# Optimization experiments

Measured on AMD Instinct MI355X. Metric: run time of the kernel, lower is better.

## Reference

```python
import jax, jax.numpy as jnp
import numpy as np

N = 50000   # nodes
E = 400000  # edges
R = 35      # num_relations
B = 12      # num_bases
C = 128     # hidden_conv_dim (heads=1)
T = 4       # node types: load, gen, load_gen, ext
HL = 38     # hidden_lin_dim
OUT = 2


def setup_inputs() -> dict:
    key = jax.random.key(0)
    ks = jax.random.split(key, 24)
    s = 0.1  # param scale
    inp = {
        'x': jax.random.normal(ks[0], (N, 2), jnp.float32),
        'edge_index': jax.random.randint(ks[1], (2, E), 0, N, jnp.int32),
        'edge_type': jax.random.randint(ks[2], (E,), 0, R, jnp.int32),
        'edge_attr': jax.random.normal(ks[3], (E, 2), jnp.float32),
        'node_type': jax.random.randint(ks[4], (N,), 0, T, jnp.int32),
        'basis': jax.random.normal(ks[5], (B, 2, C), jnp.float32) * s,
        'att_rel': jax.random.normal(ks[6], (R, B), jnp.float32) * s,
        'q_att': jax.random.normal(ks[7], (C, 1), jnp.float32) * s,
        'k_att': jax.random.normal(ks[8], (C, 1), jnp.float32) * s,
        'e_att': jax.random.normal(ks[9], (C, 1), jnp.float32) * s,
        'lin_edge_W': jax.random.normal(ks[10], (2, C), jnp.float32) * s,
        'conv_bias': jax.random.normal(ks[11], (C,), jnp.float32) * s,
        'lin0_W': jax.random.normal(ks[12], (T, C, HL), jnp.float32) * s,
        'lin0_b': jax.random.normal(ks[13], (T, HL), jnp.float32) * s,
        'lin1_W': jax.random.normal(ks[14], (T, HL, HL), jnp.float32) * s,
        'lin1_b': jax.random.normal(ks[15], (T, HL), jnp.float32) * s,
        'lin2_W': jax.random.normal(ks[16], (T, HL, HL), jnp.float32) * s,
        'lin2_b': jax.random.normal(ks[17], (T, HL), jnp.float32) * s,
        'fin_W': jax.random.normal(ks[18], (T, HL, OUT), jnp.float32) * s,
        'fin_b': jax.random.normal(ks[19], (T, OUT), jnp.float32) * s,
    }
    return inp


def _segment_softmax(alpha, dst, n):
    # PyG softmax: max is detached, eps=1e-16 on the denominator
    amax = jax.lax.stop_gradient(jax.ops.segment_max(alpha, dst, num_segments=n))
    ex = jnp.exp(alpha - amax[dst])
    den = jax.ops.segment_sum(ex, dst, num_segments=n) + 1e-16
    return ex / den[dst]


def _per_type_linear(xv, W, b, t):
    # apply node-type-specific Linear: [N,d] x [T,d,h] -> pick row type
    y = jnp.einsum('nd,tdh->nth', xv, W)              # [N,T,h]
    y = jnp.take_along_axis(y, t[:, None, None], axis=1)[:, 0]
    return y + b[t]


def reference(x, edge_index, edge_type, edge_attr, node_type,
              basis, att_rel, q_att, k_att, e_att, lin_edge_W, conv_bias,
              lin0_W, lin0_b, lin1_W, lin1_b, lin2_W, lin2_b, fin_W, fin_b):
    n = x.shape[0]
    src, dst = edge_index[0], edge_index[1]
    # RGATConv with basis decomposition: per-relation weight [R, in=2, C]
    w = jnp.einsum('rb,bio->rio', att_rel, basis)
    w_e = w[edge_type]                                 # [E,2,C] edge gather
    out_i = jnp.einsum('ei,eic->ec', x[dst], w_e)      # [E,C]
    out_j = jnp.einsum('ei,eic->ec', x[src], w_e)      # [E,C]
    ke = (edge_attr @ lin_edge_W) @ e_att              # [E,1]
    alpha = out_i @ q_att + out_j @ k_att + ke         # additive self-attention
    alpha = jax.nn.leaky_relu(alpha, 0.2)
    alpha = _segment_softmax(alpha, dst, n)            # across-relation segment softmax
    msg = alpha * out_j                                # heads=1 -> [E,C]
    agg = jax.ops.segment_sum(msg, dst, num_segments=n) + conv_bias
    h = jax.nn.leaky_relu(agg, 0.2)                    # forward activation (dropout: eval)
    t = node_type
    h = _per_type_linear(jax.nn.relu(h), lin0_W, lin0_b, t)
    h = _per_type_linear(jax.nn.relu(h), lin1_W, lin1_b, t)
    h = _per_type_linear(jax.nn.relu(h), lin2_W, lin2_b, t)
    out = _per_type_linear(h, fin_W, fin_b, t)         # [N,2]
    # load nodes (type 0): second output passes through abs
    load_out = jnp.concatenate([out[:, :1], jnp.abs(out[:, 1:2])], axis=1)
    return jnp.where((t == 0)[:, None], load_out, out)
```

## Files before the change

### kernel.cpp

```cpp
#include <hip/hip_runtime.h>
#include <math.h>

#define N_NODES 50000
#define N_EDGES 400000
#define R_REL   35
#define B_BASES 12
#define C_DIM   128
#define HL_DIM  38
#define RI2     70
#define NP      50304
#define NB_HIST 196
#define NBUCK   786
#define EPB     2048
#define CAP     704

#define OFF_WT     0
#define OFF_WQ     8960
#define OFF_WK     9030
#define OFF_LE     9100
#define OFF_META   9104
#define OFF_HBLK   9120
#define OFF_PERM   10688
#define OFF_INV    60688
#define OFF_ECUR   110992
#define OFF_EREC   111780

#define ST    0
#define WT    4760
#define HH    0
#define Y0T   0
#define Y1T   3264
#define Y2T   0
#define W1S   8192
#define W2S   9720
#define W0F   13720
#define SM_DINV 18888
#define SM_FW   18952
#define SM_FB   19028
#define LDS_FLOATS 19030

__global__ __launch_bounds__(256) void k_init(const int* __restrict__ node_type,
                                              const float* __restrict__ basis,
                                              const float* __restrict__ att_rel,
                                              const float* __restrict__ q_att,
                                              const float* __restrict__ k_att,
                                              const float* __restrict__ e_att,
                                              const float* __restrict__ lin_edge_W,
                                              float* __restrict__ ws) {
    int b = blockIdx.x, tid = threadIdx.x;
    if (b < NB_HIST) {
        __shared__ int lh[4];
        if (tid < 4) lh[tid] = 0;
        __syncthreads();
        int i = b * 256 + tid;
        if (i < N_NODES) atomicAdd(&lh[node_type[i]], 1);
        __syncthreads();
        if (tid < 4) ((int*)(ws + OFF_HBLK))[b * 4 + tid] = lh[tid];
    } else if (b < NB_HIST + 35) {
        int idx = (b - NB_HIST) * 256 + tid;
        if (idx < RI2 * C_DIM) {
            int c  = idx & (C_DIM - 1);
            int ri = idx >> 7;
            int r = ri >> 1, ii = ri & 1;
            float acc = 0.f;
            #pragma unroll
            for (int bb = 0; bb < B_BASES; ++bb)
                acc += att_rel[r * B_BASES + bb] * basis[(bb * 2 + ii) * C_DIM + c];
            ws[OFF_WT + idx] = acc;
        }
    } else if (b == NB_HIST + 35) {
        for (int i = tid; i < NBUCK; i += 256) ((int*)(ws + OFF_ECUR))[i] = 0;
    } else {
        int lane = tid & 63, wv = tid >> 6;
        int u = (b - (NB_HIST + 36)) * 4 + wv;
        if (u < 2 * RI2) {
            int ri = (u < RI2) ? u : (u - RI2);
            int r = ri >> 1, ii = ri & 1;
            const float* av = att_rel + r * B_BASES;
            const float* bs = basis + ii * C_DIM;
            float w1 = 0.f, w2 = 0.f;
            #pragma unroll
            for (int bb = 0; bb < B_BASES; ++bb) {
                float a = av[bb];
                w1 += a * bs[bb * 2 * C_DIM + lane];
                w2 += a * bs[bb * 2 * C_DIM + 64 + lane];
            }
            const float* qk = (u < RI2) ? q_att : k_att;
            float s = w1 * qk[lane] + w2 * qk[64 + lane];
            #pragma unroll
            for (int off = 32; off; off >>= 1) s += __shfl_xor(s, off, 64);
            if (lane == 0) ws[((u < RI2) ? OFF_WQ : OFF_WK) + ri] = s;
        } else if (u < 2 * RI2 + 2) {
            int j = u - 2 * RI2;
            const float* er = lin_edge_W + j * C_DIM;
            float s = er[lane] * e_att[lane] + er[64 + lane] * e_att[64 + lane];
            #pragma unroll
            for (int off = 32; off; off >>= 1) s += __shfl_xor(s, off, 64);
            if (lane == 0) ws[OFF_LE + j] = s;
        }
    }
}

__global__ __launch_bounds__(256) void k_perm(const int* __restrict__ node_type,
                                              float* __restrict__ ws) {
    __shared__ int lh[NB_HIST * 4];
    __shared__ int pre[4], tot[4], basel[4];
    __shared__ int wcnt[4][4];
    int tid = threadIdx.x;
    int lane = tid & 63, wv = tid >> 6;
    const int* hblk = (const int*)(ws + OFF_HBLK);
    for (int i = tid; i < NB_HIST * 4; i += 256) lh[i] = hblk[i];
    __syncthreads();
    if (tid < 4) {
        int run = 0, mypre = 0;
        for (int bb = 0; bb < NB_HIST; ++bb) {
            if (bb == (int)blockIdx.x) mypre = run;
            run += lh[bb * 4 + tid];
        }
        pre[tid] = mypre;
        tot[tid] = run;
    }
    __syncthreads();
    if (tid == 0) {
        int t0 = tot[0], t1 = tot[1], t2 = tot[2];
        int b1 = ((t0 + 63) >> 6) << 6;
        int b2 = b1 + (((t1 + 63) >> 6) << 6);
        int b3 = b2 + (((t2 + 63) >> 6) << 6);
        basel[0] = 0; basel[1] = b1; basel[2] = b2; basel[3] = b3;
        if (blockIdx.x == 0) {
            int* meta = (int*)(ws + OFF_META);
            meta[0] = t0; meta[1] = t1; meta[2] = t2; meta[3] = tot[3];
            meta[4] = 0;  meta[5] = b1; meta[6] = b2; meta[7] = b3;
        }
    }
    __syncthreads();
    int n = blockIdx.x * 256 + tid;
    bool active = n < N_NODES;
    int ty = active ? node_type[n] : -1;
    int myrank = 0;
    #pragma unroll
    for (int t = 0; t < 4; ++t) {
        unsigned long long m = __ballot(ty == t);
        if (lane == 0) wcnt[wv][t] = __popcll(m);
        if (ty == t) myrank = __popcll(m & ((1ULL << lane) - 1ULL));
    }
    __syncthreads();
    if (active) {
        int prew = 0;
        for (int w2 = 0; w2 < wv; ++w2) prew += wcnt[w2][ty];
        int p = basel[ty] + pre[ty] + prew + myrank;
        ((int*)(ws + OFF_PERM))[n] = p;
        ((int*)(ws + OFF_INV))[p] = n;
    }
}

__global__ __launch_bounds__(256) void k_escatter(const float* __restrict__ x,
                                                  const int* __restrict__ edge_index,
                                                  const int* __restrict__ edge_type,
                                                  const float* __restrict__ edge_attr,
                                                  float* __restrict__ ws) {
    __shared__ int hist[NBUCK];
    __shared__ int sbase[NBUCK];
    __shared__ float swq[RI2], swk[RI2], sle[2];
    int tid = threadIdx.x;
    for (int i = tid; i < NBUCK; i += 256) hist[i] = 0;
    if (tid < RI2) { swq[tid] = ws[OFF_WQ + tid]; swk[tid] = ws[OFF_WK + tid]; }
    if (tid < 2) sle[tid] = ws[OFF_LE + tid];
    __syncthreads();

    const int* perm = (const int*)(ws + OFF_PERM);
    int base = blockIdx.x * EPB;
    int   rb[8], rm[8];
    float rex[8], rsx[8], rsy[8];
    #pragma unroll
    for (int k = 0; k < 8; ++k) {
        int e = base + k * 256 + tid;
        rb[k] = -1;
        if (e < N_EDGES) {
            int src = edge_index[e];
            int dst = edge_index[N_EDGES + e];
            int r   = edge_type[e];
            int p   = perm[dst];
            float2 ea = *(const float2*)(edge_attr + 2 * e);
            float2 xs = *(const float2*)(x + 2 * src);
            float2 xd = *(const float2*)(x + 2 * dst);
            float alpha = xd.x * swq[2 * r] + xd.y * swq[2 * r + 1]
                        + xs.x * swk[2 * r] + xs.y * swk[2 * r + 1]
                        + ea.x * sle[0]     + ea.y * sle[1];
            alpha = alpha > 0.f ? alpha : 0.2f * alpha;
            float ex = __expf(alpha);
            rb[k]  = p >> 6;
            rm[k]  = (r << 6) | (p & 63);
            rex[k] = ex;
            rsx[k] = ex * xs.x;
            rsy[k] = ex * xs.y;
            atomicAdd(&hist[rb[k]], 1);
        }
    }
    __syncthreads();
    int* gcur = (int*)(ws + OFF_ECUR);
    for (int i = tid; i < NBUCK; i += 256) {
        int c = hist[i];
        sbase[i] = (c > 0) ? atomicAdd(&gcur[i], c) : 0;
    }
    __syncthreads();
    float4* rec = (float4*)(ws + OFF_EREC);
    #pragma unroll
    for (int k = 0; k < 8; ++k) {
        if (rb[k] >= 0) {
            int slot = atomicAdd(&sbase[rb[k]], 1);
            rec[(size_t)rb[k] * CAP + slot] =
                make_float4(__int_as_float(rm[k]), rex[k], rsx[k], rsy[k]);
        }
    }
}

__global__ __launch_bounds__(256) void k_node(
        const float* __restrict__ ws, const float* __restrict__ conv_bias,
        const float* __restrict__ lin0_W, const float* __restrict__ lin0_b,
        const float* __restrict__ lin1_W, const float* __restrict__ lin1_b,
        const float* __restrict__ lin2_W, const float* __restrict__ lin2_b,
        const float* __restrict__ fin_W,  const float* __restrict__ fin_b,
        float* __restrict__ out) {
    __shared__ float L[LDS_FLOATS];
    int tid  = threadIdx.x;
    int lane = tid & 63;
    int wv   = tid >> 6;
    int p0   = blockIdx.x * 64;

    const int* meta = (const int*)(ws + OFF_META);
    int b1 = meta[5], b2 = meta[6], b3 = meta[7];
    int t  = (p0 >= b1) + (p0 >= b2) + (p0 >= b3);
    int bp = meta[4 + t];
    int cnt = meta[t];

    for (int i = tid; i < RI2 * 68; i += 256) L[ST + i] = 0.f;
    if (tid < 64) L[SM_DINV + tid] = 0.f;
    if (tid >= 64 && tid < 142) {
        int i = tid - 64;
        if (i < 76) L[SM_FW + i] = fin_W[t * 76 + i];
        else        L[SM_FB + i - 76] = fin_b[t * 2 + i - 76];
    }
    const float* wT_g = ws + OFF_WT;
    for (int i4 = tid; i4 < 2240; i4 += 256) {
        float4 v = ((const float4*)wT_g)[i4];
        *(float4*)&L[WT + i4 * 4] = v;
    }
    const float* W0g = lin0_W + t * C_DIM * HL_DIM;
    for (int i = tid; i < C_DIM * HL_DIM; i += 256) {
        int cc = i / 38, j = i - cc * 38;
        L[W0F + cc * 40 + j] = W0g[i];
    }
    __syncthreads();

    {
        int ecnt = ((const int*)(ws + OFF_ECUR))[blockIdx.x];
        const float4* rec = (const float4*)(ws + OFF_EREC) + (size_t)blockIdx.x * CAP;
        for (int i = tid; i < ecnt; i += 256) {
            float4 v = rec[i];
            int m = __float_as_int(v.x);
            int n = m & 63, r = m >> 6;
            atomicAdd(&L[ST + (2 * r) * 68 + n],     v.z);
            atomicAdd(&L[ST + (2 * r + 1) * 68 + n], v.w);
            atomicAdd(&L[SM_DINV + n],               v.y);
        }
    }
    __syncthreads();
    if (tid < 64) L[SM_DINV + tid] = 1.0f / (L[SM_DINV + tid] + 1e-16f);

    int ng = lane & 15, cg_ = lane >> 4;
    int c0 = wv * 32 + cg_ * 8;
    float acc[32];
    #pragma unroll
    for (int i = 0; i < 32; ++i) acc[i] = 0.f;
    #pragma unroll 5
    for (int kk = 0; kk < RI2; ++kk) {
        float4 a4 = *(const float4*)&L[ST + kk * 68 + ng * 4];
        float4 wa = *(const float4*)&L[WT + kk * 128 + c0];
        float4 wc = *(const float4*)&L[WT + kk * 128 + c0 + 4];
        float a_[4] = {a4.x, a4.y, a4.z, a4.w};
        float w_[8] = {wa.x, wa.y, wa.z, wa.w, wc.x, wc.y, wc.z, wc.w};
        #pragma unroll
        for (int ni = 0; ni < 4; ++ni)
            #pragma unroll
            for (int ci = 0; ci < 8; ++ci)
                acc[ni * 8 + ci] += a_[ni] * w_[ci];
    }
    __syncthreads();

    {
        float4 dv = *(const float4*)&L[SM_DINV + ng * 4];
        float d_[4] = {dv.x, dv.y, dv.z, dv.w};
        #pragma unroll
        for (int ci = 0; ci < 8; ++ci) {
            float cb = conv_bias[c0 + ci];
            float4 hv;
            float h0 = acc[0 * 8 + ci] * d_[0] + cb;
            float h1 = acc[1 * 8 + ci] * d_[1] + cb;
            float h2 = acc[2 * 8 + ci] * d_[2] + cb;
            float h3 = acc[3 * 8 + ci] * d_[3] + cb;
            hv.x = h0 > 0.f ? h0 : 0.f;
            hv.y = h1 > 0.f ? h1 : 0.f;
            hv.z = h2 > 0.f ? h2 : 0.f;
            hv.w = h3 > 0.f ? h3 : 0.f;
            *(float4*)&L[HH + (c0 + ci) * 64 + ng * 4] = hv;
        }
    }
    {
        const float* W1g = lin1_W + t * HL_DIM * HL_DIM;
        const float* W2g = lin2_W + t * HL_DIM * HL_DIM;
        for (int i = tid; i < HL_DIM * HL_DIM; i += 256) {
            int cc = i / 38, j = i - cc * 38;
            L[W1S + cc * 40 + j] = W1g[i];
            L[W2S + cc * 40 + j] = W2g[i];
        }
    }
    __syncthreads();

    int jg = lane >> 4;
    int j0 = wv * 16 + jg * 4;
    float acc2[16];
    #pragma unroll
    for (int i = 0; i < 16; ++i) acc2[i] = 0.f;
    if (wv < 3) {
        #pragma unroll 4
        for (int kk = 0; kk < C_DIM; ++kk) {
            float4 a4 = *(const float4*)&L[HH + kk * 64 + ng * 4];
            float4 w4 = *(const float4*)&L[W0F + kk * 40 + j0];
            float a_[4] = {a4.x, a4.y, a4.z, a4.w};
            float w_[4] = {w4.x, w4.y, w4.z, w4.w};
            #pragma unroll
            for (int ni = 0; ni < 4; ++ni)
                #pragma unroll
                for (int ji = 0; ji < 4; ++ji)
                    acc2[ni * 4 + ji] += a_[ni] * w_[ji];
        }
    }
    __syncthreads();

    if (wv < 3) {
        #pragma unroll
        for (int ji = 0; ji < 4; ++ji) {
            int j = j0 + ji;
            float b = (j < HL_DIM) ? lin0_b[t * HL_DIM + j] : 0.f;
            float4 yv;
            float y0 = acc2[0 * 4 + ji] + b;
            float y1 = acc2[1 * 4 + ji] + b;
            float y2 = acc2[2 * 4 + ji] + b;
            float y3 = acc2[3 * 4 + ji] + b;
            yv.x = y0 > 0.f ? y0 : 0.f;
            yv.y = y1 > 0.f ? y1 : 0.f;
            yv.z = y2 > 0.f ? y2 : 0.f;
            yv.w = y3 > 0.f ? y3 : 0.f;
            *(float4*)&L[Y0T + j * 68 + ng * 4] = yv;
        }
    }
    __syncthreads();

    if (wv < 3) {
        float acc3[16];
        #pragma unroll
        for (int i = 0; i < 16; ++i) acc3[i] = 0.f;
        #pragma unroll 2
        for (int kk = 0; kk < HL_DIM; ++kk) {
            float4 a4 = *(const float4*)&L[Y0T + kk * 68 + ng * 4];
            float4 w4 = *(const float4*)&L[W1S + kk * 40 + j0];
            float a_[4] = {a4.x, a4.y, a4.z, a4.w};
            float w_[4] = {w4.x, w4.y, w4.z, w4.w};
            #pragma unroll
            for (int ni = 0; ni < 4; ++ni)
                #pragma unroll
                for (int ji = 0; ji < 4; ++ji)
                    acc3[ni * 4 + ji] += a_[ni] * w_[ji];
        }
        #pragma unroll
        for (int ji = 0; ji < 4; ++ji) {
            int j = j0 + ji;
            float b = (j < HL_DIM) ? lin1_b[t * HL_DIM + j] : 0.f;
            float4 yv;
            float y0 = acc3[0 * 4 + ji] + b;
            float y1 = acc3[1 * 4 + ji] + b;
            float y2 = acc3[2 * 4 + ji] + b;
            float y3 = acc3[3 * 4 + ji] + b;
            yv.x = y0 > 0.f ? y0 : 0.f;
            yv.y = y1 > 0.f ? y1 : 0.f;
            yv.z = y2 > 0.f ? y2 : 0.f;
            yv.w = y3 > 0.f ? y3 : 0.f;
            *(float4*)&L[Y1T + j * 68 + ng * 4] = yv;
        }
    }
    __syncthreads();

    if (wv < 3) {
        float acc4[16];
        #pragma unroll
        for (int i = 0; i < 16; ++i) acc4[i] = 0.f;
        #pragma unroll 2
        for (int kk = 0; kk < HL_DIM; ++kk) {
            float4 a4 = *(const float4*)&L[Y1T + kk * 68 + ng * 4];
            float4 w4 = *(const float4*)&L[W2S + kk * 40 + j0];
            float a_[4] = {a4.x, a4.y, a4.z, a4.w};
            float w_[4] = {w4.x, w4.y, w4.z, w4.w};
            #pragma unroll
            for (int ni = 0; ni < 4; ++ni)
                #pragma unroll
                for (int ji = 0; ji < 4; ++ji)
                    acc4[ni * 4 + ji] += a_[ni] * w_[ji];
        }
        #pragma unroll
        for (int ji = 0; ji < 4; ++ji) {
            int j = j0 + ji;
            float b = (j < HL_DIM) ? lin2_b[t * HL_DIM + j] : 0.f;
            float4 yv;
            yv.x = acc4[0 * 4 + ji] + b;
            yv.y = acc4[1 * 4 + ji] + b;
            yv.z = acc4[2 * 4 + ji] + b;
            yv.w = acc4[3 * 4 + ji] + b;
            *(float4*)&L[Y2T + j * 68 + ng * 4] = yv;
        }
    }
    __syncthreads();

    if (tid < 64) {
        int p = p0 + tid;
        bool valid = (p - bp) < cnt;
        float o0 = L[SM_FB], o1 = L[SM_FB + 1];
        for (int jj = 0; jj < HL_DIM; ++jj) {
            float v = L[Y2T + jj * 68 + tid];
            float2 f = *(const float2*)&L[SM_FW + jj * 2];
            o0 += v * f.x;
            o1 += v * f.y;
        }
        if (t == 0) o1 = fabsf(o1);
        if (valid) {
            int orig = ((const int*)(ws + OFF_INV))[p];
            ((float2*)out)[orig] = make_float2(o0, o1);
        }
    }
}

extern "C" void kernel_launch(void* const* d_in, const int* in_sizes, int n_in,
                              void* d_out, int out_size, void* d_ws, size_t ws_size,
                              hipStream_t stream) {
    const float* x          = (const float*)d_in[0];
    const int*   edge_index = (const int*)  d_in[1];
    const int*   edge_type  = (const int*)  d_in[2];
    const float* edge_attr  = (const float*)d_in[3];
    const int*   node_type  = (const int*)  d_in[4];
    const float* basis      = (const float*)d_in[5];
    const float* att_rel    = (const float*)d_in[6];
    const float* q_att      = (const float*)d_in[7];
    const float* k_att      = (const float*)d_in[8];
    const float* e_att      = (const float*)d_in[9];
    const float* lin_edge_W = (const float*)d_in[10];
    const float* conv_bias  = (const float*)d_in[11];
    const float* lin0_W     = (const float*)d_in[12];
    const float* lin0_b     = (const float*)d_in[13];
    const float* lin1_W     = (const float*)d_in[14];
    const float* lin1_b     = (const float*)d_in[15];
    const float* lin2_W     = (const float*)d_in[16];
    const float* lin2_b     = (const float*)d_in[17];
    const float* fin_W      = (const float*)d_in[18];
    const float* fin_b      = (const float*)d_in[19];

    float* ws  = (float*)d_ws;
    float* out = (float*)d_out;

    k_init    <<<NB_HIST + 35 + 1 + 36, 256, 0, stream>>>(node_type, basis, att_rel,
                                                          q_att, k_att, e_att, lin_edge_W, ws);
    k_perm    <<<NB_HIST, 256, 0, stream>>>(node_type, ws);
    k_escatter<<<NB_HIST, 256, 0, stream>>>(x, edge_index, edge_type, edge_attr, ws);
    k_node    <<<NBUCK, 256, 0, stream>>>(ws, conv_bias,
                                          lin0_W, lin0_b, lin1_W, lin1_b,
                                          lin2_W, lin2_b, fin_W, fin_b, out);
}
```

Measured before the change: 172.9 us.

## Fuse node-type permutation into setup kernel and halve edges per scatter block

Merges the per-block type histogram and permutation kernels into one: each of the 196 perm blocks redundantly scans all 50k node types to compute its own prefix and the totals, so one kernel launch and the global histogram round trip go away. The edge scatter kernel now processes 1024 edges per block over 391 blocks instead of 2048 over 196, which spreads the work across more CUs. In exchange, every perm block reads the full node_type array, adding redundant global traffic.

```diff
diff --git a/kernel.cpp b/kernel.cpp
--- a/kernel.cpp
+++ b/kernel.cpp
@@ -9,9 +9,10 @@
 #define HL_DIM  38
 #define RI2     70
 #define NP      50304
-#define NB_HIST 196
+#define NB_PERM 196
 #define NBUCK   786
-#define EPB     2048
+#define EPB     1024
+#define NBE     391
 #define CAP     704
 
 #define OFF_WT     0
@@ -19,7 +20,6 @@
 #define OFF_WK     9030
 #define OFF_LE     9100
 #define OFF_META   9104
-#define OFF_HBLK   9120
 #define OFF_PERM   10688
 #define OFF_INV    60688
 #define OFF_ECUR   110992
@@ -39,25 +39,75 @@
 #define SM_FB   19028
 #define LDS_FLOATS 19030
 
-__global__ __launch_bounds__(256) void k_init(const int* __restrict__ node_type,
-                                              const float* __restrict__ basis,
-                                              const float* __restrict__ att_rel,
-                                              const float* __restrict__ q_att,
-                                              const float* __restrict__ k_att,
-                                              const float* __restrict__ e_att,
-                                              const float* __restrict__ lin_edge_W,
-                                              float* __restrict__ ws) {
+__global__ __launch_bounds__(256) void k_setup(const int* __restrict__ node_type,
+                                               const float* __restrict__ basis,
+                                               const float* __restrict__ att_rel,
+                                               const float* __restrict__ q_att,
+                                               const float* __restrict__ k_att,
+                                               const float* __restrict__ e_att,
+                                               const float* __restrict__ lin_edge_W,
+                                               float* __restrict__ ws) {
     int b = blockIdx.x, tid = threadIdx.x;
-    if (b < NB_HIST) {
-        __shared__ int lh[4];
-        if (tid < 4) lh[tid] = 0;
+    if (b < NB_PERM) {
+        __shared__ int lh[256 * 8];
+        __shared__ int pre[4], tot[4], basel[4];
+        __shared__ int wcnt[4][4];
+        int lane = tid & 63, wv = tid >> 6;
+        int p0n = b * 256;
+        int cb0 = 0, cb1 = 0, cb2 = 0, cb3 = 0;
+        int ct0 = 0, ct1 = 0, ct2 = 0, ct3 = 0;
+        for (int i = tid; i < N_NODES; i += 256) {
+            int ty = node_type[i];
+            int below = (i < p0n) ? 1 : 0;
+            ct0 += (ty == 0); cb0 += (ty == 0) & below;
+            ct1 += (ty == 1); cb1 += (ty == 1) & below;
+            ct2 += (ty == 2); cb2 += (ty == 2) & below;
+            ct3 += (ty == 3); cb3 += (ty == 3) & below;
+        }
+        lh[tid * 8 + 0] = cb0; lh[tid * 8 + 1] = cb1;
+        lh[tid * 8 + 2] = cb2; lh[tid * 8 + 3] = cb3;
+        lh[tid * 8 + 4] = ct0; lh[tid * 8 + 5] = ct1;
+        lh[tid * 8 + 6] = ct2; lh[tid * 8 + 7] = ct3;
         __syncthreads();
-        int i = b * 256 + tid;
-        if (i < N_NODES) atomicAdd(&lh[node_type[i]], 1);
+        if (tid < 8) {
+            int s = 0;
+            for (int i = 0; i < 256; ++i) s += lh[i * 8 + tid];
+            if (tid < 4) pre[tid] = s; else tot[tid - 4] = s;
+        }
         __syncthreads();
-        if (tid < 4) ((int*)(ws + OFF_HBLK))[b * 4 + tid] = lh[tid];
-    } else if (b < NB_HIST + 35) {
-        int idx = (b - NB_HIST) * 256 + tid;
+        if (tid == 0) {
+            int t0 = tot[0], t1 = tot[1], t2 = tot[2];
+            int b1 = ((t0 + 63) >> 6) << 6;
+            int b2 = b1 + (((t1 + 63) >> 6) << 6);
+            int b3 = b2 + (((t2 + 63) >> 6) << 6);
+            basel[0] = 0; basel[1] = b1; basel[2] = b2; basel[3] = b3;
+            if (b == 0) {
+                int* meta = (int*)(ws + OFF_META);
+                meta[0] = t0; meta[1] = t1; meta[2] = t2; meta[3] = tot[3];
+                meta[4] = 0;  meta[5] = b1; meta[6] = b2; meta[7] = b3;
+            }
+        }
+        __syncthreads();
+        int n = p0n + tid;
+        bool active = n < N_NODES;
+        int ty = active ? node_type[n] : -1;
+        int myrank = 0;
+        #pragma unroll
+        for (int t = 0; t < 4; ++t) {
+            unsigned long long m = __ballot(ty == t);
+            if (lane == 0) wcnt[wv][t] = __popcll(m);
+            if (ty == t) myrank = __popcll(m & ((1ULL << lane) - 1ULL));
+        }
+        __syncthreads();
+        if (active) {
+            int prew = 0;
+            for (int w2 = 0; w2 < wv; ++w2) prew += wcnt[w2][ty];
+            int p = basel[ty] + pre[ty] + prew + myrank;
+            ((int*)(ws + OFF_PERM))[n] = p;
+            ((int*)(ws + OFF_INV))[p] = n;
+        }
+    } else if (b < NB_PERM + 35) {
+        int idx = (b - NB_PERM) * 256 + tid;
         if (idx < RI2 * C_DIM) {
             int c  = idx & (C_DIM - 1);
             int ri = idx >> 7;
@@ -68,11 +118,11 @@
                 acc += att_rel[r * B_BASES + bb] * basis[(bb * 2 + ii) * C_DIM + c];
             ws[OFF_WT + idx] = acc;
         }
-    } else if (b == NB_HIST + 35) {
+    } else if (b == NB_PERM + 35) {
         for (int i = tid; i < NBUCK; i += 256) ((int*)(ws + OFF_ECUR))[i] = 0;
     } else {
         int lane = tid & 63, wv = tid >> 6;
-        int u = (b - (NB_HIST + 36)) * 4 + wv;
+        int u = (b - (NB_PERM + 36)) * 4 + wv;
         if (u < 2 * RI2) {
             int ri = (u < RI2) ? u : (u - RI2);
             int r = ri >> 1, ii = ri & 1;
@@ -98,59 +148,6 @@
             for (int off = 32; off; off >>= 1) s += __shfl_xor(s, off, 64);
             if (lane == 0) ws[OFF_LE + j] = s;
         }
-    }
-}
-
-__global__ __launch_bounds__(256) void k_perm(const int* __restrict__ node_type,
-                                              float* __restrict__ ws) {
-    __shared__ int lh[NB_HIST * 4];
-    __shared__ int pre[4], tot[4], basel[4];
-    __shared__ int wcnt[4][4];
-    int tid = threadIdx.x;
-    int lane = tid & 63, wv = tid >> 6;
-    const int* hblk = (const int*)(ws + OFF_HBLK);
-    for (int i = tid; i < NB_HIST * 4; i += 256) lh[i] = hblk[i];
-    __syncthreads();
-    if (tid < 4) {
-        int run = 0, mypre = 0;
-        for (int bb = 0; bb < NB_HIST; ++bb) {
-            if (bb == (int)blockIdx.x) mypre = run;
-            run += lh[bb * 4 + tid];
-        }
-        pre[tid] = mypre;
-        tot[tid] = run;
-    }
-    __syncthreads();
-    if (tid == 0) {
-        int t0 = tot[0], t1 = tot[1], t2 = tot[2];
-        int b1 = ((t0 + 63) >> 6) << 6;
-        int b2 = b1 + (((t1 + 63) >> 6) << 6);
-        int b3 = b2 + (((t2 + 63) >> 6) << 6);
-        basel[0] = 0; basel[1] = b1; basel[2] = b2; basel[3] = b3;
-        if (blockIdx.x == 0) {
-            int* meta = (int*)(ws + OFF_META);
-            meta[0] = t0; meta[1] = t1; meta[2] = t2; meta[3] = tot[3];
-            meta[4] = 0;  meta[5] = b1; meta[6] = b2; meta[7] = b3;
-        }
-    }
-    __syncthreads();
-    int n = blockIdx.x * 256 + tid;
-    bool active = n < N_NODES;
-    int ty = active ? node_type[n] : -1;
-    int myrank = 0;
-    #pragma unroll
-    for (int t = 0; t < 4; ++t) {
-        unsigned long long m = __ballot(ty == t);
-        if (lane == 0) wcnt[wv][t] = __popcll(m);
-        if (ty == t) myrank = __popcll(m & ((1ULL << lane) - 1ULL));
-    }
-    __syncthreads();
-    if (active) {
-        int prew = 0;
-        for (int w2 = 0; w2 < wv; ++w2) prew += wcnt[w2][ty];
-        int p = basel[ty] + pre[ty] + prew + myrank;
-        ((int*)(ws + OFF_PERM))[n] = p;
-        ((int*)(ws + OFF_INV))[p] = n;
     }
 }
 
@@ -170,10 +167,10 @@
 
     const int* perm = (const int*)(ws + OFF_PERM);
     int base = blockIdx.x * EPB;
-    int   rb[8], rm[8];
-    float rex[8], rsx[8], rsy[8];
+    int   rb[4], rm[4];
+    float rex[4], rsx[4], rsy[4];
     #pragma unroll
-    for (int k = 0; k < 8; ++k) {
+    for (int k = 0; k < 4; ++k) {
         int e = base + k * 256 + tid;
         rb[k] = -1;
         if (e < N_EDGES) {
@@ -206,7 +203,7 @@
     __syncthreads();
     float4* rec = (float4*)(ws + OFF_EREC);
     #pragma unroll
-    for (int k = 0; k < 8; ++k) {
+    for (int k = 0; k < 4; ++k) {
         if (rb[k] >= 0) {
             int slot = atomicAdd(&sbase[rb[k]], 1);
             rec[(size_t)rb[k] * CAP + slot] =
@@ -466,10 +463,9 @@
     float* ws  = (float*)d_ws;
     float* out = (float*)d_out;
 
-    k_init    <<<NB_HIST + 35 + 1 + 36, 256, 0, stream>>>(node_type, basis, att_rel,
+    k_setup   <<<NB_PERM + 35 + 1 + 36, 256, 0, stream>>>(node_type, basis, att_rel,
                                                           q_att, k_att, e_att, lin_edge_W, ws);
-    k_perm    <<<NB_HIST, 256, 0, stream>>>(node_type, ws);
-    k_escatter<<<NB_HIST, 256, 0, stream>>>(x, edge_index, edge_type, edge_attr, ws);
+    k_escatter<<<NBE, 256, 0, stream>>>(x, edge_index, edge_type, edge_attr, ws);
     k_node    <<<NBUCK, 256, 0, stream>>>(ws, conv_bias,
                                           lin0_W, lin0_b, lin1_W, lin1_b,
                                           lin2_W, lin2_b, fin_W, fin_b, out);
```

New measurement: 205.4 us. +18.8%, slower.
